# Kernel optimization log

Measured on AMD Instinct MI355X. Metric: run time of the kernel, lower is better.

## Reference

```python
import jax, jax.numpy as jnp
import numpy as np

V, D, NH, L, HID, E, K = 32000, 1024, 16, 2, 2048, 8, 2
B, S = 2, 1024
HD = D // NH
EPS = 1e-6
ROPE_BASE = 10000.0


def setup_inputs() -> dict:
    key = jax.random.key(0)
    ks = jax.random.split(key, 12)
    s = 0.02
    return {
        "tokens": jax.random.randint(ks[0], (B, S), 0, V),
        "embed": jax.random.normal(ks[1], (V, D), jnp.float32) * s,
        "attn_norm_w": jnp.ones((L, D), jnp.float32),
        "wq": jax.random.normal(ks[2], (L, D, D), jnp.float32) * s,
        "wk": jax.random.normal(ks[3], (L, D, D), jnp.float32) * s,
        "wv": jax.random.normal(ks[4], (L, D, D), jnp.float32) * s,
        "wo": jax.random.normal(ks[5], (L, D, D), jnp.float32) * s,
        "moe_norm_w": jnp.ones((L, D), jnp.float32),
        "router_w": jax.random.normal(ks[6], (L, E, D), jnp.float32) * s,
        "w1": jax.random.normal(ks[7], (L, E, D, HID), jnp.float32) * s,
        "w2": jax.random.normal(ks[8], (L, E, HID, D), jnp.float32) * s,
        "w3": jax.random.normal(ks[9], (L, E, D, HID), jnp.float32) * s,
        "final_norm_w": jnp.ones((D,), jnp.float32),
    }


def rmsnorm(x, w):
    var = jnp.mean(jnp.square(x), axis=-1, keepdims=True)
    return x * jax.lax.rsqrt(var + EPS) * w


def rope(x):  # x: [B, S, NH, HD], rotate-half convention
    half = HD // 2
    inv = ROPE_BASE ** (-jnp.arange(half, dtype=jnp.float32) / half)
    ang = jnp.arange(x.shape[1], dtype=jnp.float32)[:, None] * inv[None, :]  # [S, half]
    cos = jnp.cos(ang)[None, :, None, :]
    sin = jnp.sin(ang)[None, :, None, :]
    x1, x2 = x[..., :half], x[..., half:]
    return jnp.concatenate([x1 * cos - x2 * sin, x1 * sin + x2 * cos], axis=-1)


def attention(x, wq, wk, wv, wo):
    q = (x @ wq).reshape(B, S, NH, HD)
    k = (x @ wk).reshape(B, S, NH, HD)
    v = (x @ wv).reshape(B, S, NH, HD)
    q, k = rope(q), rope(k)
    scores = jnp.einsum("bqhd,bkhd->bhqk", q, k) / jnp.sqrt(jnp.float32(HD))
    mask = jnp.tril(jnp.ones((S, S), bool))
    scores = jnp.where(mask[None, None], scores, jnp.finfo(scores.dtype).min)
    attn = jax.nn.softmax(scores, axis=-1)
    ctx = jnp.einsum("bhqk,bkhd->bqhd", attn, v).reshape(B, S, D)
    return ctx @ wo


def moe(x, router_w, w1, w2, w3):
    flat = x.reshape(-1, D)                      # [T, D]
    T = flat.shape[0]
    logits = flat @ router_w.T                   # [T, E]
    topv, topi = jax.lax.top_k(logits, K)
    topw = jax.nn.softmax(topv, axis=-1)         # softmax over selected logits
    gates = jnp.zeros((T, E), flat.dtype).at[jnp.arange(T)[:, None], topi].set(topw)
    out = jnp.zeros_like(flat)
    for e in range(E):  # small fixed expert count; gates are exact-sparse so math == dispatch path
        y = (jax.nn.silu(flat @ w1[e]) * (flat @ w3[e])) @ w2[e]
        out = out + y * gates[:, e:e + 1]
    return out.reshape(x.shape)


def reference(tokens, embed, attn_norm_w, wq, wk, wv, wo, moe_norm_w,
              router_w, w1, w2, w3, final_norm_w):
    x = embed[tokens]  # [B, S, D]
    for l in range(L):
        x = x + attention(rmsnorm(x, attn_norm_w[l]), wq[l], wk[l], wv[l], wo[l])
        x = x + moe(rmsnorm(x, moe_norm_w[l]), router_w[l], w1[l], w2[l], w3[l])
    x = rmsnorm(x, final_norm_w)
    return x @ embed.T  # tied logits [B, S, V]
```

## Files before the change

### kernel.cpp

```cpp
#include <hip/hip_runtime.h>
#include <math.h>

typedef unsigned short u16;
typedef unsigned int u32;
typedef __attribute__((ext_vector_type(8))) short bf16x8;
typedef __attribute__((ext_vector_type(4))) float f32x4;

#define TOK 2048
#define SEQ 1024
#define DM 1024
#define NEXP 8
#define VOCAB 32000
#define NL 2
#define SLOTS 5120
#define APAD 40

__device__ __forceinline__ float bf2f(u16 v) {
  u32 u = ((u32)v) << 16; float f; __builtin_memcpy(&f, &u, 4); return f;
}
__device__ __forceinline__ u16 f2bf(float f) {
  u32 u; __builtin_memcpy(&u, &f, 4);
  u += 0x7fffu + ((u >> 16) & 1u);
  return (u16)(u >> 16);
}
__device__ __forceinline__ void split8(const float* v, u16* hi, u16* lo) {
#pragma unroll
  for (int j = 0; j < 8; j++) {
    hi[j] = f2bf(v[j]);
    lo[j] = f2bf(v[j] - bf2f(hi[j]));
  }
}

__global__ __launch_bounds__(256) void k_f2bf(const float* __restrict__ in,
                                              u16* __restrict__ out, long n4) {
  long i = (long)blockIdx.x * 256 + threadIdx.x;
  long stride = (long)gridDim.x * 256;
  for (; i < n4; i += stride) {
    float4 v = ((const float4*)in)[i];
    ushort4 o;
    o.x = f2bf(v.x); o.y = f2bf(v.y); o.z = f2bf(v.z); o.w = f2bf(v.w);
    ((ushort4*)out)[i] = o;
  }
}

__device__ __forceinline__ void norm_emit_hl(float4 v, const float* __restrict__ w,
    u16* __restrict__ ohi, u16* __restrict__ olo, int t) {
  float ss = v.x * v.x + v.y * v.y + v.z * v.z + v.w * v.w;
  for (int off = 32; off; off >>= 1) ss += __shfl_xor(ss, off);
  __shared__ float red[4];
  if ((threadIdx.x & 63) == 0) red[threadIdx.x >> 6] = ss;
  __syncthreads();
  float tot = red[0] + red[1] + red[2] + red[3];
  float sc = rsqrtf(tot * (1.0f / 1024.0f) + 1e-6f);
  float4 wv = ((const float4*)w)[threadIdx.x];
  float o[4] = {v.x * sc * wv.x, v.y * sc * wv.y, v.z * sc * wv.z, v.w * sc * wv.w};
  ushort4 hi, lo;
  hi.x = f2bf(o[0]); lo.x = f2bf(o[0] - bf2f(hi.x));
  hi.y = f2bf(o[1]); lo.y = f2bf(o[1] - bf2f(hi.y));
  hi.z = f2bf(o[2]); lo.z = f2bf(o[2] - bf2f(hi.z));
  hi.w = f2bf(o[3]); lo.w = f2bf(o[3] - bf2f(hi.w));
  ((ushort4*)(ohi + (long)t * DM))[threadIdx.x] = hi;
  ((ushort4*)(olo + (long)t * DM))[threadIdx.x] = lo;
}
__device__ __forceinline__ void norm_emit_b(float4 v, const float* __restrict__ w,
    u16* __restrict__ out, int t) {
  float ss = v.x * v.x + v.y * v.y + v.z * v.z + v.w * v.w;
  for (int off = 32; off; off >>= 1) ss += __shfl_xor(ss, off);
  __shared__ float red[4];
  if ((threadIdx.x & 63) == 0) red[threadIdx.x >> 6] = ss;
  __syncthreads();
  float tot = red[0] + red[1] + red[2] + red[3];
  float sc = rsqrtf(tot * (1.0f / 1024.0f) + 1e-6f);
  float4 wv = ((const float4*)w)[threadIdx.x];
  ushort4 o;
  o.x = f2bf(v.x * sc * wv.x); o.y = f2bf(v.y * sc * wv.y);
  o.z = f2bf(v.z * sc * wv.z); o.w = f2bf(v.w * sc * wv.w);
  ((ushort4*)(out + (long)t * DM))[threadIdx.x] = o;
}

__global__ __launch_bounds__(256) void k_gather_norm(const int* __restrict__ tok,
    const float* __restrict__ embed, const float* __restrict__ w,
    float* __restrict__ x, u16* __restrict__ ohi, u16* __restrict__ olo,
    int* __restrict__ counts) {
  int t = blockIdx.x;
  if (t == 0 && threadIdx.x < NEXP) counts[threadIdx.x] = 0;
  float4 v = ((const float4*)(embed + (long)tok[t] * DM))[threadIdx.x];
  ((float4*)(x + (long)t * DM))[threadIdx.x] = v;
  norm_emit_hl(v, w, ohi, olo, t);
}

#define KP 72
#define VP 40
#define PP 36
__global__ __launch_bounds__(256) void k_attn(const u16* __restrict__ qhi,
    const u16* __restrict__ qlo, u16* __restrict__ chi, u16* __restrict__ clo) {
  __shared__ u16 Ksh[32 * KP], Ksl[32 * KP];
  __shared__ u16 Vsh[64 * VP], Vsl[64 * VP];
  __shared__ float Ps[4][16 * PP];
  int bid = blockIdx.x;
  int xcd = bid & 7, r = bid >> 3;
  int bh = xcd * 4 + (r >> 4);
  int qt = 15 - (r & 15);
  int b = bh >> 4, h = bh & 15;
  int tid = threadIdx.x, w = tid >> 6, lane = tid & 63;
  int lrow = lane & 15, lgrp = lane >> 4;
  int q0 = qt * 64;
  long qrow = (long)(b * SEQ + q0 + w * 16 + lrow);
  bf16x8 qh[2], ql[2];
#pragma unroll
  for (int dsl = 0; dsl < 2; dsl++) {
    long off = qrow * 3072 + h * 64 + dsl * 32 + lgrp * 8;
    qh[dsl] = *(const bf16x8*)(qhi + off);
    ql[dsl] = *(const bf16x8*)(qlo + off);
  }
  f32x4 cacc[4] = {};
  float mst[4], lst[4];
#pragma unroll
  for (int j = 0; j < 4; j++) { mst[j] = -__builtin_inff(); lst[j] = 0.0f; }
  int srow = tid >> 3, dchunk = (tid & 7) * 8;
  for (int s0 = 0; s0 < q0 + 64; s0 += 32) {
    long kvrow = (long)(b * SEQ + s0 + srow) * 3072 + h * 64;
    {
      *(uint4*)(Ksh + srow * KP + dchunk) = *(const uint4*)(qhi + kvrow + 1024 + dchunk);
      *(uint4*)(Ksl + srow * KP + dchunk) = *(const uint4*)(qlo + kvrow + 1024 + dchunk);
      uint4 hv4 = *(const uint4*)(qhi + kvrow + 2048 + dchunk);
      uint4 lv4 = *(const uint4*)(qlo + kvrow + 2048 + dchunk);
      const u16* hp = (const u16*)&hv4;
      const u16* lp = (const u16*)&lv4;
#pragma unroll
      for (int j = 0; j < 8; j++) {
        Vsh[(dchunk + j) * VP + srow] = hp[j];
        Vsl[(dchunk + j) * VP + srow] = lp[j];
      }
    }
    __syncthreads();
    f32x4 sacc[2] = {};
#pragma unroll
    for (int sf = 0; sf < 2; sf++)
#pragma unroll
      for (int dsl = 0; dsl < 2; dsl++) {
        bf16x8 kh = *(const bf16x8*)(Ksh + (sf * 16 + lrow) * KP + dsl * 32 + lgrp * 8);
        bf16x8 kl = *(const bf16x8*)(Ksl + (sf * 16 + lrow) * KP + dsl * 32 + lgrp * 8);
        sacc[sf] = __builtin_amdgcn_mfma_f32_16x16x32_bf16(qh[dsl], kh, sacc[sf], 0, 0, 0);
        sacc[sf] = __builtin_amdgcn_mfma_f32_16x16x32_bf16(qh[dsl], kl, sacc[sf], 0, 0, 0);
        sacc[sf] = __builtin_amdgcn_mfma_f32_16x16x32_bf16(ql[dsl], kh, sacc[sf], 0, 0, 0);
      }
#pragma unroll
    for (int sf = 0; sf < 2; sf++)
#pragma unroll
      for (int j = 0; j < 4; j++) {
        int col = s0 + sf * 16 + lrow;
        int row = q0 + w * 16 + lgrp * 4 + j;
        float v = sacc[sf][j] * 0.125f;
        sacc[sf][j] = (col <= row) ? v : -1e30f;
      }
    float fac[4];
#pragma unroll
    for (int j = 0; j < 4; j++) {
      float mx = fmaxf(sacc[0][j], sacc[1][j]);
      for (int off = 1; off < 16; off <<= 1) mx = fmaxf(mx, __shfl_xor(mx, off));
      float mnew = fmaxf(mst[j], mx);
      float f = __expf(mst[j] - mnew);
      mst[j] = mnew;
      float p0 = __expf(sacc[0][j] - mnew);
      float p1 = __expf(sacc[1][j] - mnew);
      sacc[0][j] = p0; sacc[1][j] = p1;
      float ps = p0 + p1;
      for (int off = 1; off < 16; off <<= 1) ps += __shfl_xor(ps, off);
      lst[j] = lst[j] * f + ps;
      fac[j] = f;
    }
#pragma unroll
    for (int n = 0; n < 4; n++)
#pragma unroll
      for (int j = 0; j < 4; j++) cacc[n][j] *= fac[j];
#pragma unroll
    for (int sf = 0; sf < 2; sf++)
#pragma unroll
      for (int j = 0; j < 4; j++)
        Ps[w][(lgrp * 4 + j) * PP + sf * 16 + lrow] = sacc[sf][j];
    float pv[8];
#pragma unroll
    for (int j = 0; j < 8; j++) pv[j] = Ps[w][lrow * PP + lgrp * 8 + j];
    u16 phi[8], plo[8];
    split8(pv, phi, plo);
    bf16x8 ph = *(bf16x8*)phi, pl = *(bf16x8*)plo;
#pragma unroll
    for (int n = 0; n < 4; n++) {
      bf16x8 vh = *(const bf16x8*)(Vsh + (n * 16 + lrow) * VP + lgrp * 8);
      bf16x8 vl = *(const bf16x8*)(Vsl + (n * 16 + lrow) * VP + lgrp * 8);
      cacc[n] = __builtin_amdgcn_mfma_f32_16x16x32_bf16(ph, vh, cacc[n], 0, 0, 0);
      cacc[n] = __builtin_amdgcn_mfma_f32_16x16x32_bf16(ph, vl, cacc[n], 0, 0, 0);
      cacc[n] = __builtin_amdgcn_mfma_f32_16x16x32_bf16(pl, vh, cacc[n], 0, 0, 0);
    }
    __syncthreads();
  }
#pragma unroll
  for (int n = 0; n < 4; n++)
#pragma unroll
    for (int j = 0; j < 4; j++) {
      long t = (long)(b * SEQ + q0 + w * 16 + lgrp * 4 + j);
      float v = cacc[n][j] / lst[j];
      u16 hv = f2bf(v);
      chi[t * DM + h * 64 + n * 16 + lrow] = hv;
      clo[t * DM + h * 64 + n * 16 + lrow] = f2bf(v - bf2f(hv));
    }
}


__device__ __forceinline__ void stageB_tr(const float* __restrict__ B, int ldb,
    int k0, int n0, u16* Bh, u16* Bl, int tid, int split) {
#pragma unroll
  for (int ph = 0; ph < 2; ph++) {
    int c = tid + 256 * ph;
    int nr = c & 127;
    int ks = c >> 7;
    const float* src = B + (long)(k0 + ks * 8) * ldb + n0 + nr;
    float v[8];
#pragma unroll
    for (int j = 0; j < 8; j++) v[j] = src[(long)j * ldb];
    u16 hi[8];
#pragma unroll
    for (int j = 0; j < 8; j++) hi[j] = f2bf(v[j]);
    *(uint4*)(Bh + nr * APAD + ks * 8) = *(uint4*)hi;
    if (split) {
      u16 lo[8];
#pragma unroll
      for (int j = 0; j < 8; j++) lo[j] = f2bf(v[j] - bf2f(hi[j]));
      *(uint4*)(Bl + nr * APAD + ks * 8) = *(uint4*)lo;
    }
  }
}

__global__ __launch_bounds__(256) void k_wo(
    const u16* __restrict__ Ahi, const u16* __restrict__ Alo,
    const float* __restrict__ B, float* __restrict__ C) {
  __shared__ u16 Ah[64 * APAD], Al[64 * APAD], Bh[128 * APAD], Bl[128 * APAD];
  int bid = blockIdx.x;
  int n0 = (bid & 7) * 128;
  int m0 = (bid >> 3) * 64;
  int tid = threadIdx.x, lane = tid & 63, w = tid >> 6;
  int wr = w >> 1, wc = w & 1, lrow = lane & 15, lgrp = lane >> 4;
  f32x4 acc[2][4] = {};
  for (int k0 = 0; k0 < 1024; k0 += 32) {
    {
      int row = tid >> 2, kc = tid & 3;
      long off = (long)(m0 + row) * DM + k0 + kc * 8;
      *(uint4*)(Ah + row * APAD + kc * 8) = *(const uint4*)(Ahi + off);
      *(uint4*)(Al + row * APAD + kc * 8) = *(const uint4*)(Alo + off);
    }
    stageB_tr(B, 1024, k0, n0, Bh, Bl, tid, 1);
    __syncthreads();
    bf16x8 ah[2], al[2], bh[4], bl[4];
#pragma unroll
    for (int i = 0; i < 2; i++) {
      ah[i] = *(const bf16x8*)(Ah + (wr * 32 + i * 16 + lrow) * APAD + lgrp * 8);
      al[i] = *(const bf16x8*)(Al + (wr * 32 + i * 16 + lrow) * APAD + lgrp * 8);
    }
#pragma unroll
    for (int j = 0; j < 4; j++) {
      bh[j] = *(const bf16x8*)(Bh + (wc * 64 + j * 16 + lrow) * APAD + lgrp * 8);
      bl[j] = *(const bf16x8*)(Bl + (wc * 64 + j * 16 + lrow) * APAD + lgrp * 8);
    }
#pragma unroll
    for (int i = 0; i < 2; i++)
#pragma unroll
      for (int j = 0; j < 4; j++) {
        acc[i][j] = __builtin_amdgcn_mfma_f32_16x16x32_bf16(ah[i], bh[j], acc[i][j], 0, 0, 0);
        acc[i][j] = __builtin_amdgcn_mfma_f32_16x16x32_bf16(ah[i], bl[j], acc[i][j], 0, 0, 0);
        acc[i][j] = __builtin_amdgcn_mfma_f32_16x16x32_bf16(al[i], bh[j], acc[i][j], 0, 0, 0);
      }
    __syncthreads();
  }
#pragma unroll
  for (int i = 0; i < 2; i++)
#pragma unroll
    for (int j = 0; j < 4; j++) {
      int col = n0 + wc * 64 + j * 16 + lrow;
#pragma unroll
      for (int jj = 0; jj < 4; jj++) {
        int r = m0 + wr * 32 + i * 16 + lgrp * 4 + jj;
        C[(long)r * DM + col] += acc[i][j][jj];
      }
    }
}

__global__ __launch_bounds__(256) void k_gemm_qkv(
    const u16* __restrict__ Ahi, const u16* __restrict__ Alo,
    const float* __restrict__ Bq, const float* __restrict__ Bk,
    const float* __restrict__ Bv, u16* __restrict__ Chi, u16* __restrict__ Clo) {
  __shared__ u16 Ah[64 * APAD], Al[64 * APAD], Bh[128 * APAD], Bl[128 * APAD];
  int bid = blockIdx.x;
  int xcd = bid & 7, r = bid >> 3;
  int nb = xcd * 3 + r / 32;
  int m0 = (r & 31) * 64;
  const float* B = (nb < 8) ? Bq : (nb < 16) ? Bk : Bv;
  int bn0 = (nb & 7) * 128;
  int tid = threadIdx.x, lane = tid & 63, w = tid >> 6;
  int wr = w >> 1, wc = w & 1, lrow = lane & 15, lgrp = lane >> 4;
  f32x4 acc[2][4] = {};
  for (int k0 = 0; k0 < 1024; k0 += 32) {
    {
      int row = tid >> 2, kc = tid & 3;
      long off = (long)(m0 + row) * DM + k0 + kc * 8;
      *(uint4*)(Ah + row * APAD + kc * 8) = *(const uint4*)(Ahi + off);
      *(uint4*)(Al + row * APAD + kc * 8) = *(const uint4*)(Alo + off);
    }
    stageB_tr(B, 1024, k0, bn0, Bh, Bl, tid, 1);
    __syncthreads();
    bf16x8 ah[2], al[2], bh[4], bl[4];
#pragma unroll
    for (int i = 0; i < 2; i++) {
      ah[i] = *(const bf16x8*)(Ah + (wr * 32 + i * 16 + lrow) * APAD + lgrp * 8);
      al[i] = *(const bf16x8*)(Al + (wr * 32 + i * 16 + lrow) * APAD + lgrp * 8);
    }
#pragma unroll
    for (int j = 0; j < 4; j++) {
      bh[j] = *(const bf16x8*)(Bh + (wc * 64 + j * 16 + lrow) * APAD + lgrp * 8);
      bl[j] = *(const bf16x8*)(Bl + (wc * 64 + j * 16 + lrow) * APAD + lgrp * 8);
    }
#pragma unroll
    for (int i = 0; i < 2; i++)
#pragma unroll
      for (int j = 0; j < 4; j++) {
        acc[i][j] = __builtin_amdgcn_mfma_f32_16x16x32_bf16(ah[i], bh[j], acc[i][j], 0, 0, 0);
        acc[i][j] = __builtin_amdgcn_mfma_f32_16x16x32_bf16(ah[i], bl[j], acc[i][j], 0, 0, 0);
        acc[i][j] = __builtin_amdgcn_mfma_f32_16x16x32_bf16(al[i], bh[j], acc[i][j], 0, 0, 0);
      }
    __syncthreads();
  }
  if (nb < 16) {
    float inv1 = exp2f((float)lrow * (-13.287712379549449f / 32.0f));
    float inv2 = exp2f((float)(lrow + 16) * (-13.287712379549449f / 32.0f));
#pragma unroll
    for (int i = 0; i < 2; i++)
#pragma unroll
      for (int jj = 0; jj < 4; jj++) {
        int rr = m0 + wr * 32 + i * 16 + lgrp * 4 + jj;
        float s = (float)(rr & (SEQ - 1));
        float sn1, cs1, sn2, cs2;
        sincosf(s * inv1, &sn1, &cs1);
        sincosf(s * inv2, &sn2, &cs2);
        float q1 = acc[i][0][jj], q2 = acc[i][2][jj];
        acc[i][0][jj] = q1 * cs1 - q2 * sn1;
        acc[i][2][jj] = q1 * sn1 + q2 * cs1;
        float p1 = acc[i][1][jj], p2 = acc[i][3][jj];
        acc[i][1][jj] = p1 * cs2 - p2 * sn2;
        acc[i][3][jj] = p1 * sn2 + p2 * cs2;
      }
  }
#pragma unroll
  for (int i = 0; i < 2; i++)
#pragma unroll
    for (int j = 0; j < 4; j++) {
      int col = nb * 128 + wc * 64 + j * 16 + lrow;
#pragma unroll
      for (int jj = 0; jj < 4; jj++) {
        int rr = m0 + wr * 32 + i * 16 + lgrp * 4 + jj;
        float v = acc[i][j][jj];
        u16 hv = f2bf(v);
        Chi[(long)rr * 3072 + col] = hv;
        Clo[(long)rr * 3072 + col] = f2bf(v - bf2f(hv));
      }
    }
}

template <int SPLIT>
__global__ __launch_bounds__(256) void k_w13(
    const u16* __restrict__ Ahi, const u16* __restrict__ Alo,
    const float* __restrict__ W1, const float* __restrict__ W3,
    const int* __restrict__ lists, const int* __restrict__ counts,
    const int* __restrict__ aoff,
    float* __restrict__ h13) {
  int bid = blockIdx.x;
  int xcd = bid & 7, r = bid >> 3;
  int nb = xcd * 4 + r / 80;
  int m0 = (r % 80) * 64;
  int e = -1;
#pragma unroll
  for (int i = 0; i < NEXP; i++)
    if (m0 >= aoff[i] && m0 < aoff[i + 1]) e = i;
  if (e < 0) return;
  int lr0 = m0 - aoff[e];
  int Mc = counts[e];
  if (lr0 >= Mc) return;
  const float* B = ((nb < 16) ? W1 : W3) + (size_t)e * 1024 * 2048;
  int bn0 = (nb & 15) * 128;
  const int* lst = lists + e * TOK;
  __shared__ u16 Ah[64 * APAD], Bh[128 * APAD];
  __shared__ u16 Al[SPLIT ? 64 * APAD : 1], Bl[SPLIT ? 128 * APAD : 1];
  int tid = threadIdx.x, lane = tid & 63, w = tid >> 6;
  int wr = w >> 1, wc = w & 1, lrow = lane & 15, lgrp = lane >> 4;
  f32x4 acc[2][4] = {};
  for (int k0 = 0; k0 < 1024; k0 += 32) {
    {
      int row = tid >> 2, kc = tid & 3;
      uint4 vh = make_uint4(0, 0, 0, 0), vl = make_uint4(0, 0, 0, 0);
      if (lr0 + row < Mc) {
        long off = (long)lst[lr0 + row] * DM + k0 + kc * 8;
        vh = *(const uint4*)(Ahi + off);
        if (SPLIT) vl = *(const uint4*)(Alo + off);
      }
      *(uint4*)(Ah + row * APAD + kc * 8) = vh;
      if (SPLIT) *(uint4*)(Al + row * APAD + kc * 8) = vl;
    }
    stageB_tr(B, 2048, k0, bn0, Bh, Bl, tid, SPLIT);
    __syncthreads();
    bf16x8 ah[2], bh[4];
#pragma unroll
    for (int i = 0; i < 2; i++)
      ah[i] = *(const bf16x8*)(Ah + (wr * 32 + i * 16 + lrow) * APAD + lgrp * 8);
#pragma unroll
    for (int j = 0; j < 4; j++)
      bh[j] = *(const bf16x8*)(Bh + (wc * 64 + j * 16 + lrow) * APAD + lgrp * 8);
#pragma unroll
    for (int i = 0; i < 2; i++)
#pragma unroll
      for (int j = 0; j < 4; j++)
        acc[i][j] = __builtin_amdgcn_mfma_f32_16x16x32_bf16(ah[i], bh[j], acc[i][j], 0, 0, 0);
    if (SPLIT) {
      bf16x8 al[2], bl[4];
#pragma unroll
      for (int i = 0; i < 2; i++)
        al[i] = *(const bf16x8*)(Al + (wr * 32 + i * 16 + lrow) * APAD + lgrp * 8);
#pragma unroll
      for (int j = 0; j < 4; j++)
        bl[j] = *(const bf16x8*)(Bl + (wc * 64 + j * 16 + lrow) * APAD + lgrp * 8);
#pragma unroll
      for (int i = 0; i < 2; i++)
#pragma unroll
        for (int j = 0; j < 4; j++) {
          acc[i][j] = __builtin_amdgcn_mfma_f32_16x16x32_bf16(ah[i], bl[j], acc[i][j], 0, 0, 0);
          acc[i][j] = __builtin_amdgcn_mfma_f32_16x16x32_bf16(al[i], bh[j], acc[i][j], 0, 0, 0);
        }
    }
    __syncthreads();
  }
#pragma unroll
  for (int i = 0; i < 2; i++)
#pragma unroll
    for (int j = 0; j < 4; j++) {
      int col = nb * 128 + wc * 64 + j * 16 + lrow;
#pragma unroll
      for (int jj = 0; jj < 4; jj++) {
        int rl = wr * 32 + i * 16 + lgrp * 4 + jj;
        if (lr0 + rl >= Mc) continue;
        h13[(long)(m0 + rl) * 4096 + col] = acc[i][j][jj];
      }
    }
}

__global__ __launch_bounds__(256) void k_silu(const float* __restrict__ h13,
    const int* __restrict__ counts, const int* __restrict__ aoff,
    u16* __restrict__ hhi, u16* __restrict__ hlo) {
  int g = blockIdx.x;
  int e = -1;
#pragma unroll
  for (int i = 0; i < NEXP; i++)
    if (g >= aoff[i] && g < aoff[i + 1]) e = i;
  if (e < 0 || g - aoff[e] >= counts[e]) return;
  const float4* a = (const float4*)(h13 + (long)g * 4096);
  const float4* b = (const float4*)(h13 + (long)g * 4096 + 2048);
  for (int c = threadIdx.x; c < 512; c += 256) {
    float4 x1 = a[c], x3 = b[c];
    float o[4];
    o[0] = x1.x / (1.0f + __expf(-x1.x)) * x3.x;
    o[1] = x1.y / (1.0f + __expf(-x1.y)) * x3.y;
    o[2] = x1.z / (1.0f + __expf(-x1.z)) * x3.z;
    o[3] = x1.w / (1.0f + __expf(-x1.w)) * x3.w;
    ushort4 hi, lo;
    hi.x = f2bf(o[0]); lo.x = f2bf(o[0] - bf2f(hi.x));
    hi.y = f2bf(o[1]); lo.y = f2bf(o[1] - bf2f(hi.y));
    hi.z = f2bf(o[2]); lo.z = f2bf(o[2] - bf2f(hi.z));
    hi.w = f2bf(o[3]); lo.w = f2bf(o[3] - bf2f(hi.w));
    ((ushort4*)(hhi + (long)g * 2048))[c] = hi;
    ((ushort4*)(hlo + (long)g * 2048))[c] = lo;
  }
}

template <int SPLIT>
__global__ __launch_bounds__(256) void k_w2(
    const u16* __restrict__ Ahi, const u16* __restrict__ Alo,
    const float* __restrict__ W2,
    const int* __restrict__ counts, const int* __restrict__ aoff,
    float* __restrict__ y) {
  int bid = blockIdx.x;
  int n0 = (bid & 7) * 128;
  int m0 = (bid >> 3) * 64;
  int e = -1;
#pragma unroll
  for (int i = 0; i < NEXP; i++)
    if (m0 >= aoff[i] && m0 < aoff[i + 1]) e = i;
  if (e < 0) return;
  int lr0 = m0 - aoff[e];
  int Mc = counts[e];
  if (lr0 >= Mc) return;
  const float* B = W2 + (size_t)e * 2048 * 1024;
  __shared__ u16 Ah[64 * APAD], Bh[128 * APAD];
  __shared__ u16 Al[SPLIT ? 64 * APAD : 1], Bl[SPLIT ? 128 * APAD : 1];
  int tid = threadIdx.x, lane = tid & 63, w = tid >> 6;
  int wr = w >> 1, wc = w & 1, lrow = lane & 15, lgrp = lane >> 4;
  f32x4 acc[2][4] = {};
  for (int k0 = 0; k0 < 2048; k0 += 32) {
    {
      int row = tid >> 2, kc = tid & 3;
      long off = (long)(m0 + row) * 2048 + k0 + kc * 8;
      *(uint4*)(Ah + row * APAD + kc * 8) = *(const uint4*)(Ahi + off);
      if (SPLIT) *(uint4*)(Al + row * APAD + kc * 8) = *(const uint4*)(Alo + off);
    }
    stageB_tr(B, 1024, k0, n0, Bh, Bl, tid, SPLIT);
    __syncthreads();
    bf16x8 ah[2], bh[4];
#pragma unroll
    for (int i = 0; i < 2; i++)
      ah[i] = *(const bf16x8*)(Ah + (wr * 32 + i * 16 + lrow) * APAD + lgrp * 8);
#pragma unroll
    for (int j = 0; j < 4; j++)
      bh[j] = *(const bf16x8*)(Bh + (wc * 64 + j * 16 + lrow) * APAD + lgrp * 8);
#pragma unroll
    for (int i = 0; i < 2; i++)
#pragma unroll
      for (int j = 0; j < 4; j++)
        acc[i][j] = __builtin_amdgcn_mfma_f32_16x16x32_bf16(ah[i], bh[j], acc[i][j], 0, 0, 0);
    if (SPLIT) {
      bf16x8 al[2], bl[4];
#pragma unroll
      for (int i = 0; i < 2; i++)
        al[i] = *(const bf16x8*)(Al + (wr * 32 + i * 16 + lrow) * APAD + lgrp * 8);
#pragma unroll
      for (int j = 0; j < 4; j++)
        bl[j] = *(const bf16x8*)(Bl + (wc * 64 + j * 16 + lrow) * APAD + lgrp * 8);
#pragma unroll
      for (int i = 0; i < 2; i++)
#pragma unroll
        for (int j = 0; j < 4; j++) {
          acc[i][j] = __builtin_amdgcn_mfma_f32_16x16x32_bf16(ah[i], bl[j], acc[i][j], 0, 0, 0);
          acc[i][j] = __builtin_amdgcn_mfma_f32_16x16x32_bf16(al[i], bh[j], acc[i][j], 0, 0, 0);
        }
    }
    __syncthreads();
  }
#pragma unroll
  for (int i = 0; i < 2; i++)
#pragma unroll
    for (int j = 0; j < 4; j++) {
      int col = n0 + wc * 64 + j * 16 + lrow;
#pragma unroll
      for (int jj = 0; jj < 4; jj++) {
        int rl = wr * 32 + i * 16 + lgrp * 4 + jj;
        if (lr0 + rl >= Mc) continue;
        y[(long)(m0 + rl) * DM + col] = acc[i][j][jj];
      }
    }
}

template <int FINAL>
__global__ __launch_bounds__(256) void k_combine_norm(const float* __restrict__ y,
    const int* __restrict__ aoff, const int* __restrict__ tok_e,
    const int* __restrict__ tok_pos, const float* __restrict__ tok_gate,
    float* __restrict__ x, const float* __restrict__ wnext,
    u16* __restrict__ ohi, u16* __restrict__ olo, int* __restrict__ counts) {
  int t = blockIdx.x;
  if (!FINAL && t == 0 && threadIdx.x < NEXP) counts[threadIdx.x] = 0;
  float4 acc = ((float4*)(x + (long)t * DM))[threadIdx.x];
#pragma unroll
  for (int j = 0; j < 2; j++) {
    int e = tok_e[t * 2 + j];
    long g = aoff[e] + tok_pos[t * 2 + j];
    float gt = tok_gate[t * 2 + j];
    float4 yv = ((const float4*)(y + g * DM))[threadIdx.x];
    acc.x += gt * yv.x; acc.y += gt * yv.y;
    acc.z += gt * yv.z; acc.w += gt * yv.w;
  }
  ((float4*)(x + (long)t * DM))[threadIdx.x] = acc;
  if (FINAL) norm_emit_b(acc, wnext, ohi, t);
  else norm_emit_hl(acc, wnext, ohi, olo, t);
}

__device__ __forceinline__ void logits_mma(const u16* As, const u16* Bs,
    f32x4 (&acc)[4][4], int wr, int wc, int lrow, int lgrp) {
  bf16x8 af[4], bfr[4];
#pragma unroll
  for (int i = 0; i < 4; i++) {
    af[i] = *(const bf16x8*)(As + (wr * 64 + i * 16 + lrow) * APAD + lgrp * 8);
    bfr[i] = *(const bf16x8*)(Bs + (wc * 64 + i * 16 + lrow) * APAD + lgrp * 8);
  }
#pragma unroll
  for (int i = 0; i < 4; i++)
#pragma unroll
    for (int j = 0; j < 4; j++)
      acc[i][j] = __builtin_amdgcn_mfma_f32_16x16x32_bf16(af[i], bfr[j], acc[i][j], 0, 0, 0);
}

__global__ __launch_bounds__(512) void k_logits(
    const u16* __restrict__ A, const u16* __restrict__ Bt,
    float* __restrict__ C) {
  __shared__ u16 AsA[256 * APAD], BsA[128 * APAD];
  __shared__ u16 AsB[256 * APAD], BsB[128 * APAD];
  int bid = blockIdx.x;
  int xcd = bid & 7, rank = bid >> 3;
  int bx = xcd * 32 + (rank >> 3);
  int by = rank & 7;
  if (bx >= VOCAB / 128) return;
  int m0 = by * 256, n0 = bx * 128;
  int tid = threadIdx.x, lane = tid & 63, w = tid >> 6;
  int wr = w >> 1, wc = w & 1;
  int lrow = lane & 15, lgrp = lane >> 4;
  int arow = tid >> 2, akc = tid & 3;
  f32x4 acc[4][4] = {};
  const u16* Ap = A + (long)(m0 + arow) * 1024 + akc * 8;
  const u16* Ap2 = A + (long)(m0 + arow + 128) * 1024 + akc * 8;
  const u16* Bp = Bt + (long)(n0 + arow) * 1024 + akc * 8;
  uint4 a0 = *(const uint4*)(Ap);
  uint4 a1 = *(const uint4*)(Ap2);
  uint4 b0 = *(const uint4*)(Bp);
  *(uint4*)(AsA + arow * APAD + akc * 8) = a0;
  *(uint4*)(AsA + (arow + 128) * APAD + akc * 8) = a1;
  *(uint4*)(BsA + arow * APAD + akc * 8) = b0;
  __syncthreads();
  for (int kt = 0; kt < 32; kt += 2) {
    {
      int k0 = (kt + 1) * 32;
      a0 = *(const uint4*)(Ap + k0);
      a1 = *(const uint4*)(Ap2 + k0);
      b0 = *(const uint4*)(Bp + k0);
    }
    logits_mma(AsA, BsA, acc, wr, wc, lrow, lgrp);
    *(uint4*)(AsB + arow * APAD + akc * 8) = a0;
    *(uint4*)(AsB + (arow + 128) * APAD + akc * 8) = a1;
    *(uint4*)(BsB + arow * APAD + akc * 8) = b0;
    __syncthreads();
    if (kt + 2 < 32) {
      int k0 = (kt + 2) * 32;
      a0 = *(const uint4*)(Ap + k0);
      a1 = *(const uint4*)(Ap2 + k0);
      b0 = *(const uint4*)(Bp + k0);
    }
    logits_mma(AsB, BsB, acc, wr, wc, lrow, lgrp);
    if (kt + 2 < 32) {
      *(uint4*)(AsA + arow * APAD + akc * 8) = a0;
      *(uint4*)(AsA + (arow + 128) * APAD + akc * 8) = a1;
      *(uint4*)(BsA + arow * APAD + akc * 8) = b0;
    }
    __syncthreads();
  }
#pragma unroll
  for (int i = 0; i < 4; i++)
#pragma unroll
    for (int j = 0; j < 4; j++) {
      int col = n0 + wc * 64 + j * 16 + lrow;
#pragma unroll
      for (int jj = 0; jj < 4; jj++) {
        int r = m0 + wr * 64 + i * 16 + lgrp * 4 + jj;
        C[(long)r * VOCAB + col] = acc[i][j][jj];
      }
    }
}

__global__ __launch_bounds__(256) void k_router_norm(const float* __restrict__ x,
    const float* __restrict__ nw, const float* __restrict__ rw,
    int* __restrict__ counts, int* __restrict__ lists,
    int* __restrict__ tok_e, int* __restrict__ tok_pos,
    float* __restrict__ tok_gate,
    u16* __restrict__ ohi, u16* __restrict__ olo) {
  int t = blockIdx.x * 4 + (threadIdx.x >> 6);
  int lane = threadIdx.x & 63;
  const float* xr = x + (long)t * DM;
  float xv[16], wv[16];
  float ss = 0.0f;
  float p[8] = {0, 0, 0, 0, 0, 0, 0, 0};
#pragma unroll
  for (int i = 0; i < 16; i++) {
    int d = lane + 64 * i;
    xv[i] = xr[d];
    wv[i] = nw[d];
    ss += xv[i] * xv[i];
    float xw = xv[i] * wv[i];
#pragma unroll
    for (int e = 0; e < 8; e++) p[e] += xw * rw[e * DM + d];
  }
  for (int off = 32; off; off >>= 1) ss += __shfl_xor(ss, off);
#pragma unroll
  for (int e = 0; e < 8; e++)
    for (int off = 32; off; off >>= 1) p[e] += __shfl_xor(p[e], off);
  float sc = rsqrtf(ss * (1.0f / 1024.0f) + 1e-6f);
#pragma unroll
  for (int i = 0; i < 16; i++) {
    int d = lane + 64 * i;
    float o = xv[i] * sc * wv[i];
    u16 h = f2bf(o);
    ohi[(long)t * DM + d] = h;
    olo[(long)t * DM + d] = f2bf(o - bf2f(h));
  }
  if (lane == 0) {
    int e0 = 0, e1 = -1;
    float v0 = -__builtin_inff(), v1 = -__builtin_inff();
    for (int e = 0; e < 8; e++) {
      float pe = p[e] * sc;
      if (pe > v0) { v1 = v0; e1 = e0; v0 = pe; e0 = e; }
      else if (pe > v1) { v1 = pe; e1 = e; }
    }
    float w0 = 1.0f / (1.0f + expf(v1 - v0));
    int pos0 = atomicAdd(&counts[e0], 1);
    lists[e0 * TOK + pos0] = t;
    tok_e[t * 2] = e0; tok_pos[t * 2] = pos0; tok_gate[t * 2] = w0;
    int pos1 = atomicAdd(&counts[e1], 1);
    lists[e1 * TOK + pos1] = t;
    tok_e[t * 2 + 1] = e1; tok_pos[t * 2 + 1] = pos1; tok_gate[t * 2 + 1] = 1.0f - w0;
  }
}

__global__ void k_offsets(const int* __restrict__ counts, int* __restrict__ aoff) {
  if (threadIdx.x == 0 && blockIdx.x == 0) {
    int a = 0;
    for (int e = 0; e < NEXP; e++) {
      aoff[e] = a;
      a += (counts[e] + 63) & ~63;
    }
    aoff[NEXP] = a;
  }
}

extern "C" void kernel_launch(void* const* d_in, const int* in_sizes, int n_in,
                              void* d_out, int out_size, void* d_ws, size_t ws_size,
                              hipStream_t stream) {
  (void)in_sizes; (void)n_in; (void)out_size; (void)ws_size;
  const int* tokens = (const int*)d_in[0];
  const float* embed = (const float*)d_in[1];
  const float* attn_nw = (const float*)d_in[2];
  const float* wq = (const float*)d_in[3];
  const float* wk = (const float*)d_in[4];
  const float* wv = (const float*)d_in[5];
  const float* wo = (const float*)d_in[6];
  const float* moe_nw = (const float*)d_in[7];
  const float* rw = (const float*)d_in[8];
  const float* w1 = (const float*)d_in[9];
  const float* w2 = (const float*)d_in[10];
  const float* w3 = (const float*)d_in[11];
  const float* fin_nw = (const float*)d_in[12];
  float* out = (float*)d_out;

  char* ob = (char*)d_out;
  auto carve = [&](size_t bytes) { char* r = ob; ob += (bytes + 255) & ~(size_t)255; return r; };
  u16*   qkv_hi = (u16*)carve((size_t)TOK * 3072 * 2);
  u16*   qkv_lo = (u16*)carve((size_t)TOK * 3072 * 2);
  u16*   ctx_hi = (u16*)carve((size_t)TOK * DM * 2);
  u16*   ctx_lo = (u16*)carve((size_t)TOK * DM * 2);
  float* x      = (float*)carve((size_t)TOK * DM * 4);
  float* h13    = (float*)carve((size_t)SLOTS * 4096 * 4);
  u16*   hb_hi  = (u16*)carve((size_t)SLOTS * 2048 * 2);
  u16*   hb_lo  = (u16*)carve((size_t)SLOTS * 2048 * 2);
  float* y      = (float*)carve((size_t)SLOTS * 1024 * 4);
  int*   counts  = (int*)carve(NEXP * 4);
  int*   aoff    = (int*)carve((NEXP + 1) * 4);
  int*   lists   = (int*)carve((size_t)NEXP * TOK * 4);
  int*   tok_e   = (int*)carve((size_t)TOK * 2 * 4);
  int*   tok_pos = (int*)carve((size_t)TOK * 2 * 4);
  float* tok_gate= (float*)carve((size_t)TOK * 2 * 4);
  char* wp = (char*)d_ws;
  auto wcarve = [&](size_t bytes) { char* r = wp; wp += (bytes + 255) & ~(size_t)255; return r; };
  u16* xn_hi = (u16*)wcarve((size_t)TOK * DM * 2);
  u16* xn_lo = (u16*)wcarve((size_t)TOK * DM * 2);
  u16* xnb   = (u16*)wcarve((size_t)TOK * DM * 2);
  u16* embB  = (u16*)wcarve((size_t)VOCAB * DM * 2);

  k_f2bf<<<4096, 256, 0, stream>>>(embed, embB, (long)VOCAB * DM / 4);
  k_gather_norm<<<TOK, 256, 0, stream>>>(tokens, embed, attn_nw, x, xn_hi, xn_lo, counts);

  for (int l = 0; l < NL; l++) {
    k_gemm_qkv<<<768, 256, 0, stream>>>(xn_hi, xn_lo,
        wq + (size_t)l * DM * DM, wk + (size_t)l * DM * DM, wv + (size_t)l * DM * DM,
        qkv_hi, qkv_lo);
    k_attn<<<512, 256, 0, stream>>>(qkv_hi, qkv_lo, ctx_hi, ctx_lo);
    k_wo<<<256, 256, 0, stream>>>(ctx_hi, ctx_lo, wo + (size_t)l * DM * DM, x);

    k_router_norm<<<TOK / 4, 256, 0, stream>>>(x, moe_nw + (size_t)l * DM,
        rw + (size_t)l * NEXP * DM, counts, lists, tok_e, tok_pos, tok_gate,
        xn_hi, xn_lo);
    k_offsets<<<1, 64, 0, stream>>>(counts, aoff);
    if (l < NL - 1) {
      k_w13<1><<<2560, 256, 0, stream>>>(xn_hi, xn_lo,
          w1 + (size_t)l * NEXP * DM * 2048, w3 + (size_t)l * NEXP * DM * 2048,
          lists, counts, aoff, h13);
      k_silu<<<SLOTS, 256, 0, stream>>>(h13, counts, aoff, hb_hi, hb_lo);
      k_w2<1><<<640, 256, 0, stream>>>(hb_hi, hb_lo,
          w2 + (size_t)l * NEXP * 2048 * DM, counts, aoff, y);
      k_combine_norm<0><<<TOK, 256, 0, stream>>>(y, aoff, tok_e, tok_pos, tok_gate,
          x, attn_nw + (size_t)(l + 1) * DM, xn_hi, xn_lo, counts);
    } else {
      k_w13<0><<<2560, 256, 0, stream>>>(xn_hi, xn_lo,
          w1 + (size_t)l * NEXP * DM * 2048, w3 + (size_t)l * NEXP * DM * 2048,
          lists, counts, aoff, h13);
      k_silu<<<SLOTS, 256, 0, stream>>>(h13, counts, aoff, hb_hi, hb_lo);
      k_w2<0><<<640, 256, 0, stream>>>(hb_hi, hb_lo,
          w2 + (size_t)l * NEXP * 2048 * DM, counts, aoff, y);
      k_combine_norm<1><<<TOK, 256, 0, stream>>>(y, aoff, tok_e, tok_pos, tok_gate,
          x, fin_nw, xnb, nullptr, nullptr);
    }
  }
  k_logits<<<2048, 512, 0, stream>>>(xnb, embB, out);
}
```

Before: 1.270 ms.

## Fuse SiLU-gating into W1/W3 GEMM, computing both projections per block

Each k_w13 block now stages both W1 and W3 tiles and keeps two accumulator sets, so the SiLU(x·W1)·(x·W3) product is formed in registers and written straight out as bf16 hi/lo. This removes the fp32 h13 intermediate (SLOTS×4096 floats) and the separate k_silu launch, saving a full write and read of that buffer. The grid is halved, and each block uses roughly twice the shared memory and accumulator registers, which may lower occupancy.

New measurement: 1.251 ms. No clear change (-1.6%).

```diff
diff --git a/kernel.cpp b/kernel.cpp
--- a/kernel.cpp
+++ b/kernel.cpp
@@ -371,10 +371,10 @@
     const float* __restrict__ W1, const float* __restrict__ W3,
     const int* __restrict__ lists, const int* __restrict__ counts,
     const int* __restrict__ aoff,
-    float* __restrict__ h13) {
+    u16* __restrict__ hhi, u16* __restrict__ hlo) {
   int bid = blockIdx.x;
   int xcd = bid & 7, r = bid >> 3;
-  int nb = xcd * 4 + r / 80;
+  int nb = xcd * 2 + r / 80;
   int m0 = (r % 80) * 64;
   int e = -1;
 #pragma unroll
@@ -384,14 +384,16 @@
   int lr0 = m0 - aoff[e];
   int Mc = counts[e];
   if (lr0 >= Mc) return;
-  const float* B = ((nb < 16) ? W1 : W3) + (size_t)e * 1024 * 2048;
-  int bn0 = (nb & 15) * 128;
+  const float* B1 = W1 + (size_t)e * 1024 * 2048;
+  const float* B3 = W3 + (size_t)e * 1024 * 2048;
+  int bn0 = nb * 128;
   const int* lst = lists + e * TOK;
-  __shared__ u16 Ah[64 * APAD], Bh[128 * APAD];
-  __shared__ u16 Al[SPLIT ? 64 * APAD : 1], Bl[SPLIT ? 128 * APAD : 1];
+  __shared__ u16 Ah[64 * APAD], B1h[128 * APAD], B3h[128 * APAD];
+  __shared__ u16 Al[SPLIT ? 64 * APAD : 1];
+  __shared__ u16 B1l[SPLIT ? 128 * APAD : 1], B3l[SPLIT ? 128 * APAD : 1];
   int tid = threadIdx.x, lane = tid & 63, w = tid >> 6;
   int wr = w >> 1, wc = w & 1, lrow = lane & 15, lgrp = lane >> 4;
-  f32x4 acc[2][4] = {};
+  f32x4 acc1[2][4] = {}, acc3[2][4] = {};
   for (int k0 = 0; k0 < 1024; k0 += 32) {
     {
       int row = tid >> 2, kc = tid & 3;
@@ -404,35 +406,62 @@
       *(uint4*)(Ah + row * APAD + kc * 8) = vh;
       if (SPLIT) *(uint4*)(Al + row * APAD + kc * 8) = vl;
     }
-    stageB_tr(B, 2048, k0, bn0, Bh, Bl, tid, SPLIT);
-    __syncthreads();
-    bf16x8 ah[2], bh[4];
-#pragma unroll
-    for (int i = 0; i < 2; i++)
+    stageB_tr(B1, 2048, k0, bn0, B1h, B1l, tid, SPLIT);
+    stageB_tr(B3, 2048, k0, bn0, B3h, B3l, tid, SPLIT);
+    __syncthreads();
+    bf16x8 ah[2], al[2];
+#pragma unroll
+    for (int i = 0; i < 2; i++) {
       ah[i] = *(const bf16x8*)(Ah + (wr * 32 + i * 16 + lrow) * APAD + lgrp * 8);
-#pragma unroll
-    for (int j = 0; j < 4; j++)
-      bh[j] = *(const bf16x8*)(Bh + (wc * 64 + j * 16 + lrow) * APAD + lgrp * 8);
-#pragma unroll
-    for (int i = 0; i < 2; i++)
+      if (SPLIT) al[i] = *(const bf16x8*)(Al + (wr * 32 + i * 16 + lrow) * APAD + lgrp * 8);
+    }
+    {
+      bf16x8 bh[4];
 #pragma unroll
       for (int j = 0; j < 4; j++)
-        acc[i][j] = __builtin_amdgcn_mfma_f32_16x16x32_bf16(ah[i], bh[j], acc[i][j], 0, 0, 0);
-    if (SPLIT) {
-      bf16x8 al[2], bl[4];
+        bh[j] = *(const bf16x8*)(B1h + (wc * 64 + j * 16 + lrow) * APAD + lgrp * 8);
 #pragma unroll
       for (int i = 0; i < 2; i++)
-        al[i] = *(const bf16x8*)(Al + (wr * 32 + i * 16 + lrow) * APAD + lgrp * 8);
+#pragma unroll
+        for (int j = 0; j < 4; j++)
+          acc1[i][j] = __builtin_amdgcn_mfma_f32_16x16x32_bf16(ah[i], bh[j], acc1[i][j], 0, 0, 0);
+      if (SPLIT) {
+        bf16x8 bl[4];
+#pragma unroll
+        for (int j = 0; j < 4; j++)
+          bl[j] = *(const bf16x8*)(B1l + (wc * 64 + j * 16 + lrow) * APAD + lgrp * 8);
+#pragma unroll
+        for (int i = 0; i < 2; i++)
+#pragma unroll
+          for (int j = 0; j < 4; j++) {
+            acc1[i][j] = __builtin_amdgcn_mfma_f32_16x16x32_bf16(ah[i], bl[j], acc1[i][j], 0, 0, 0);
+            acc1[i][j] = __builtin_amdgcn_mfma_f32_16x16x32_bf16(al[i], bh[j], acc1[i][j], 0, 0, 0);
+          }
+      }
+    }
+    {
+      bf16x8 bh[4];
 #pragma unroll
       for (int j = 0; j < 4; j++)
-        bl[j] = *(const bf16x8*)(Bl + (wc * 64 + j * 16 + lrow) * APAD + lgrp * 8);
+        bh[j] = *(const bf16x8*)(B3h + (wc * 64 + j * 16 + lrow) * APAD + lgrp * 8);
 #pragma unroll
       for (int i = 0; i < 2; i++)
 #pragma unroll
-        for (int j = 0; j < 4; j++) {
-          acc[i][j] = __builtin_amdgcn_mfma_f32_16x16x32_bf16(ah[i], bl[j], acc[i][j], 0, 0, 0);
-          acc[i][j] = __builtin_amdgcn_mfma_f32_16x16x32_bf16(al[i], bh[j], acc[i][j], 0, 0, 0);
-        }
+        for (int j = 0; j < 4; j++)
+          acc3[i][j] = __builtin_amdgcn_mfma_f32_16x16x32_bf16(ah[i], bh[j], acc3[i][j], 0, 0, 0);
+      if (SPLIT) {
+        bf16x8 bl[4];
+#pragma unroll
+        for (int j = 0; j < 4; j++)
+          bl[j] = *(const bf16x8*)(B3l + (wc * 64 + j * 16 + lrow) * APAD + lgrp * 8);
+#pragma unroll
+        for (int i = 0; i < 2; i++)
+#pragma unroll
+          for (int j = 0; j < 4; j++) {
+            acc3[i][j] = __builtin_amdgcn_mfma_f32_16x16x32_bf16(ah[i], bl[j], acc3[i][j], 0, 0, 0);
+            acc3[i][j] = __builtin_amdgcn_mfma_f32_16x16x32_bf16(al[i], bh[j], acc3[i][j], 0, 0, 0);
+          }
+      }
     }
     __syncthreads();
   }
@@ -440,42 +469,18 @@
   for (int i = 0; i < 2; i++)
 #pragma unroll
     for (int j = 0; j < 4; j++) {
-      int col = nb * 128 + wc * 64 + j * 16 + lrow;
+      int col = bn0 + wc * 64 + j * 16 + lrow;
 #pragma unroll
       for (int jj = 0; jj < 4; jj++) {
         int rl = wr * 32 + i * 16 + lgrp * 4 + jj;
         if (lr0 + rl >= Mc) continue;
-        h13[(long)(m0 + rl) * 4096 + col] = acc[i][j][jj];
-      }
-    }
-}
-
-__global__ __launch_bounds__(256) void k_silu(const float* __restrict__ h13,
-    const int* __restrict__ counts, const int* __restrict__ aoff,
-    u16* __restrict__ hhi, u16* __restrict__ hlo) {
-  int g = blockIdx.x;
-  int e = -1;
-#pragma unroll
-  for (int i = 0; i < NEXP; i++)
-    if (g >= aoff[i] && g < aoff[i + 1]) e = i;
-  if (e < 0 || g - aoff[e] >= counts[e]) return;
-  const float4* a = (const float4*)(h13 + (long)g * 4096);
-  const float4* b = (const float4*)(h13 + (long)g * 4096 + 2048);
-  for (int c = threadIdx.x; c < 512; c += 256) {
-    float4 x1 = a[c], x3 = b[c];
-    float o[4];
-    o[0] = x1.x / (1.0f + __expf(-x1.x)) * x3.x;
-    o[1] = x1.y / (1.0f + __expf(-x1.y)) * x3.y;
-    o[2] = x1.z / (1.0f + __expf(-x1.z)) * x3.z;
-    o[3] = x1.w / (1.0f + __expf(-x1.w)) * x3.w;
-    ushort4 hi, lo;
-    hi.x = f2bf(o[0]); lo.x = f2bf(o[0] - bf2f(hi.x));
-    hi.y = f2bf(o[1]); lo.y = f2bf(o[1] - bf2f(hi.y));
-    hi.z = f2bf(o[2]); lo.z = f2bf(o[2] - bf2f(hi.z));
-    hi.w = f2bf(o[3]); lo.w = f2bf(o[3] - bf2f(hi.w));
-    ((ushort4*)(hhi + (long)g * 2048))[c] = hi;
-    ((ushort4*)(hlo + (long)g * 2048))[c] = lo;
-  }
+        float g = acc1[i][j][jj], u = acc3[i][j][jj];
+        float o = g / (1.0f + __expf(-g)) * u;
+        u16 hv = f2bf(o);
+        hhi[(long)(m0 + rl) * 2048 + col] = hv;
+        if (SPLIT) hlo[(long)(m0 + rl) * 2048 + col] = f2bf(o - bf2f(hv));
+      }
+    }
 }
 
 template <int SPLIT>
@@ -747,7 +752,6 @@
   u16*   ctx_hi = (u16*)carve((size_t)TOK * DM * 2);
   u16*   ctx_lo = (u16*)carve((size_t)TOK * DM * 2);
   float* x      = (float*)carve((size_t)TOK * DM * 4);
-  float* h13    = (float*)carve((size_t)SLOTS * 4096 * 4);
   u16*   hb_hi  = (u16*)carve((size_t)SLOTS * 2048 * 2);
   u16*   hb_lo  = (u16*)carve((size_t)SLOTS * 2048 * 2);
   float* y      = (float*)carve((size_t)SLOTS * 1024 * 4);
@@ -779,19 +783,17 @@
         xn_hi, xn_lo);
     k_offsets<<<1, 64, 0, stream>>>(counts, aoff);
     if (l < NL - 1) {
-      k_w13<1><<<2560, 256, 0, stream>>>(xn_hi, xn_lo,
+      k_w13<1><<<1280, 256, 0, stream>>>(xn_hi, xn_lo,
           w1 + (size_t)l * NEXP * DM * 2048, w3 + (size_t)l * NEXP * DM * 2048,
-          lists, counts, aoff, h13);
-      k_silu<<<SLOTS, 256, 0, stream>>>(h13, counts, aoff, hb_hi, hb_lo);
+          lists, counts, aoff, hb_hi, hb_lo);
       k_w2<1><<<640, 256, 0, stream>>>(hb_hi, hb_lo,
           w2 + (size_t)l * NEXP * 2048 * DM, counts, aoff, y);
       k_combine_norm<0><<<TOK, 256, 0, stream>>>(y, aoff, tok_e, tok_pos, tok_gate,
           x, attn_nw + (size_t)(l + 1) * DM, xn_hi, xn_lo, counts);
     } else {
-      k_w13<0><<<2560, 256, 0, stream>>>(xn_hi, xn_lo,
+      k_w13<0><<<1280, 256, 0, stream>>>(xn_hi, xn_lo,
           w1 + (size_t)l * NEXP * DM * 2048, w3 + (size_t)l * NEXP * DM * 2048,
-          lists, counts, aoff, h13);
-      k_silu<<<SLOTS, 256, 0, stream>>>(h13, counts, aoff, hb_hi, hb_lo);
+          lists, counts, aoff, hb_hi, nullptr);
       k_w2<0><<<640, 256, 0, stream>>>(hb_hi, hb_lo,
           w2 + (size_t)l * NEXP * 2048 * DM, counts, aoff, y);
       k_combine_norm<1><<<TOK, 256, 0, stream>>>(y, aoff, tok_e, tok_pos, tok_gate,
```
